# Performance work log

Measured on AMD Instinct MI355X. Metric: run time of the kernel, lower is better.

## Reference

```python
import jax, jax.numpy as jnp
import numpy as np

N_NODES = 50000
N_EDGES = 600000
N_GRAPHS = 100
IN_DIM, HID, OUT = 128, 128, 64
K = 2  # DGL TAGConv default hop count


def setup_inputs() -> dict:
    key = jax.random.key(0)
    ks = jax.random.split(key, 8)
    x = jax.random.normal(ks[0], (N_NODES, IN_DIM), dtype=jnp.float32)
    src = jax.random.randint(ks[1], (N_EDGES,), 0, N_NODES)
    dst = jax.random.randint(ks[2], (N_EDGES,), 0, N_NODES)
    graph_id = jnp.sort(jax.random.randint(ks[3], (N_NODES,), 0, N_GRAPHS))
    # TAGConv lin: Linear(in_feats*(K+1), out_feats), stored as (in*(K+1), out)
    W1 = jax.random.normal(ks[4], (IN_DIM * (K + 1), HID), dtype=jnp.float32) / np.sqrt(IN_DIM * (K + 1))
    b1 = jnp.zeros((HID,), dtype=jnp.float32)
    W2 = jax.random.normal(ks[5], (HID * (K + 1), OUT), dtype=jnp.float32) / np.sqrt(HID * (K + 1))
    b2 = jnp.zeros((OUT,), dtype=jnp.float32)
    return {"x": x, "W1": W1, "b1": b1, "W2": W2, "b2": b2,
            "src": src, "dst": dst, "graph_id": graph_id}


def _tagconv(h, src, dst, norm, W, b):
    """DGL TAGConv: relu(concat_k (D^-1/2 A D^-1/2)^k h @ W + b), k=0..K."""
    feats = [h]
    cur = h
    for _ in range(K):
        cur = cur * norm[:, None]
        cur = jax.ops.segment_sum(cur[src], dst, num_segments=N_NODES)
        cur = cur * norm[:, None]
        feats.append(cur)
    out = jnp.concatenate(feats, axis=-1) @ W + b
    return jax.nn.relu(out)


def reference(x, W1, b1, W2, b2, src, dst, graph_id):
    # symmetric norm from in-degrees (clamped to 1), as in DGL TAGConv
    deg = jax.ops.segment_sum(jnp.ones_like(dst, dtype=x.dtype), dst, num_segments=N_NODES)
    norm = jnp.clip(deg, 1.0, None) ** -0.5
    h = _tagconv(x, src, dst, norm, W1, b1)
    h = _tagconv(h, src, dst, norm, W2, b2)
    # MaxPooling readout: per-graph max over nodes
    return jax.ops.segment_max(h, graph_id, num_segments=N_GRAPHS)
```

## Files before the change

### kernel.cpp

```cpp
#include <hip/hip_runtime.h>
#include <hip/hip_bf16.h>

#define N_NODES 50000
#define N_EDGES 600000
#define N_GRAPHS 100
#define M_PAD 50176

typedef __bf16 bf16_t;
typedef __attribute__((ext_vector_type(8))) __bf16 bf16x8;
typedef __attribute__((ext_vector_type(2))) __bf16 bf16x2;
typedef __attribute__((ext_vector_type(4))) float f32x4;

__global__ void degk(const int* __restrict__ dst, int* __restrict__ deg, int n) {
    int i = blockIdx.x * 256 + threadIdx.x;
    if (i < n) atomicAdd(&deg[dst[i]], 1);
}

__global__ __launch_bounds__(1024) void scan1(const int* __restrict__ deg,
                                              int* __restrict__ row_off,
                                              int* __restrict__ partial,
                                              float* __restrict__ norm, int n) {
    __shared__ int buf[1024];
    int i = blockIdx.x * 1024 + threadIdx.x;
    int v = (i < n) ? deg[i] : 0;
    if (i < n) norm[i] = rsqrtf(fmaxf((float)v, 1.0f));
    buf[threadIdx.x] = v;
    __syncthreads();
    for (int off = 1; off < 1024; off <<= 1) {
        int t = (threadIdx.x >= off) ? buf[threadIdx.x - off] : 0;
        __syncthreads();
        buf[threadIdx.x] += t;
        __syncthreads();
    }
    if (i < n) row_off[i + 1] = buf[threadIdx.x];
    if (threadIdx.x == 1023) partial[blockIdx.x] = buf[1023];
}

__global__ void scan2(int* __restrict__ partial, int nchunks) {
    int lane = threadIdx.x;
    int v = (lane < nchunks) ? partial[lane] : 0;
    for (int off = 1; off < 64; off <<= 1) {
        int t = __shfl_up(v, off, 64);
        if (lane >= off) v += t;
    }
    int ex = __shfl_up(v, 1, 64);
    if (lane == 0) ex = 0;
    if (lane < nchunks) partial[lane] = ex;
}

__global__ void scan3(int* __restrict__ row_off, const int* __restrict__ partial, int n) {
    int i = blockIdx.x * 256 + threadIdx.x;
    if (i == 0) row_off[0] = 0;
    if (i < n) row_off[i + 1] += partial[i >> 10];
}

__global__ void scatterk(const int* __restrict__ src, const int* __restrict__ dst,
                         const int* __restrict__ row_off, int* __restrict__ cursor,
                         int* __restrict__ csr_src, int n) {
    int e = blockIdx.x * 256 + threadIdx.x;
    if (e >= n) return;
    int d = dst[e];
    int pos = atomicAdd(&cursor[d], 1);
    csr_src[row_off[d] + pos] = src[e];
}

__global__ void prescale(const float* __restrict__ x, bf16_t* __restrict__ xb, int n) {
    int i = blockIdx.x * 256 + threadIdx.x;
    if (i >= n * 64) return;
    int node = i >> 6;
    int c = (i & 63) * 2;
    float2 v = *(const float2*)(x + (size_t)node * 128 + c);
    bf16x2 vb; vb[0] = (bf16_t)v.x; vb[1] = (bf16_t)v.y;
    *(bf16x2*)(xb + (size_t)node * 128 + c) = vb;
}

__global__ void permWall(const float* __restrict__ W1, const float* __restrict__ W2,
                         bf16_t* __restrict__ Wp1, bf16_t* __restrict__ Wp2) {
    int i = blockIdx.x * 256 + threadIdx.x;
    const float* W; bf16_t* Wp; int N;
    if (i < 384 * 128) { W = W1; Wp = Wp1; N = 128; }
    else if (i < 384 * 128 + 384 * 64) { i -= 384 * 128; W = W2; Wp = Wp2; N = 64; }
    else return;
    int k = i / N, n = i - k * N;
    int kt = k >> 5, q = (k >> 3) & 3, j = k & 7;
    int nt = n >> 4, ln = n & 15;
    int lane = q * 16 + ln;
    Wp[(((size_t)kt * (N >> 4) + nt) * 64 + lane) * 8 + j] = (bf16_t)W[i];
}

__global__ __launch_bounds__(256) void spmm3(const bf16_t* __restrict__ in,
                                             bf16_t* __restrict__ out,
                                             const float* __restrict__ norm,
                                             const int* __restrict__ row_off,
                                             const int* __restrict__ csr_src, int n) {
    int sub = threadIdx.x >> 4;
    int l   = threadIdx.x & 15;
    int node = blockIdx.x * 16 + sub;
    if (node >= n) return;
    const bf16_t* colp = in + l * 8;
    int e0 = row_off[node], e1 = row_off[node + 1];
    float acc[8] = {};
    int e = e0;
    for (; e + 8 <= e1; e += 8) {
        int s[8];
#pragma unroll
        for (int u = 0; u < 8; u++) s[u] = csr_src[e + u];
        bf16x8 v[8];
#pragma unroll
        for (int u = 0; u < 8; u++) v[u] = *(const bf16x8*)(colp + (size_t)s[u] * 128);
        float ns[8];
#pragma unroll
        for (int u = 0; u < 8; u++) ns[u] = norm[s[u]];
#pragma unroll
        for (int u = 0; u < 8; u++)
#pragma unroll
            for (int j = 0; j < 8; j++) acc[j] += ns[u] * (float)v[u][j];
    }
    for (; e + 4 <= e1; e += 4) {
        int s[4];
#pragma unroll
        for (int u = 0; u < 4; u++) s[u] = csr_src[e + u];
        bf16x8 v[4];
#pragma unroll
        for (int u = 0; u < 4; u++) v[u] = *(const bf16x8*)(colp + (size_t)s[u] * 128);
        float ns[4];
#pragma unroll
        for (int u = 0; u < 4; u++) ns[u] = norm[s[u]];
#pragma unroll
        for (int u = 0; u < 4; u++)
#pragma unroll
            for (int j = 0; j < 8; j++) acc[j] += ns[u] * (float)v[u][j];
    }
    for (; e < e1; e++) {
        int s = csr_src[e];
        float ns = norm[s];
        bf16x8 v = *(const bf16x8*)(colp + (size_t)s * 128);
#pragma unroll
        for (int j = 0; j < 8; j++) acc[j] += ns * (float)v[j];
    }
    float nd = norm[node];
    bf16x8 o;
#pragma unroll
    for (int j = 0; j < 8; j++) o[j] = (bf16_t)(acc[j] * nd);
    *(bf16x8*)(out + (size_t)node * 128 + l * 8) = o;
}

template <int NT, bool BF16OUT>
__global__ __launch_bounds__(256) void gemm_mfma(const bf16_t* __restrict__ f0,
                                                 const bf16_t* __restrict__ f1,
                                                 const bf16_t* __restrict__ f2,
                                                 const bf16_t* __restrict__ Wp,
                                                 const float* __restrict__ bias,
                                                 bf16_t* __restrict__ out_b,
                                                 float* __restrict__ out_f, int M) {
    int wave = threadIdx.x >> 6;
    int lane = threadIdx.x & 63;
    int q = lane >> 4, ln = lane & 15;
    int row0 = blockIdx.x * 128 + wave * 32;

    f32x4 acc[2][NT] = {};
    const bf16_t* feats[3] = {f0, f1, f2};
    const bf16x8* Wf = (const bf16x8*)Wp;

#pragma unroll
    for (int kc = 0; kc < 12; kc++) {
        const bf16_t* A = feats[kc >> 2] + (size_t)(kc & 3) * 32 + q * 8;
        bf16x8 a0 = *(const bf16x8*)(A + (size_t)(row0 + ln) * 128);
        bf16x8 a1 = *(const bf16x8*)(A + (size_t)(row0 + 16 + ln) * 128);
        const bf16x8* Bp = Wf + (size_t)kc * NT * 64 + lane;
#pragma unroll
        for (int nt = 0; nt < NT; nt++) {
            bf16x8 b = Bp[nt * 64];
            acc[0][nt] = __builtin_amdgcn_mfma_f32_16x16x32_bf16(a0, b, acc[0][nt], 0, 0, 0);
            acc[1][nt] = __builtin_amdgcn_mfma_f32_16x16x32_bf16(a1, b, acc[1][nt], 0, 0, 0);
        }
    }

    float bv[NT];
#pragma unroll
    for (int nt = 0; nt < NT; nt++) bv[nt] = bias[nt * 16 + ln];

#pragma unroll
    for (int mt = 0; mt < 2; mt++) {
#pragma unroll
        for (int r = 0; r < 4; r++) {
            int row = row0 + mt * 16 + q * 4 + r;
            if (row >= M) continue;
#pragma unroll
            for (int nt = 0; nt < NT; nt++) {
                int col = nt * 16 + ln;
                float val = fmaxf(acc[mt][nt][r] + bv[nt], 0.f);
                if (BF16OUT) out_b[(size_t)row * 128 + col] = (bf16_t)val;
                else         out_f[(size_t)row * 64 + col] = val;
            }
        }
    }
}

__global__ __launch_bounds__(256) void maxpool2(const float* __restrict__ hF,
                                                const int* __restrict__ gid,
                                                unsigned int* __restrict__ out, int n) {
    int wave = threadIdx.x >> 6;
    int lane = threadIdx.x & 63;
    int n0 = blockIdx.x * 256 + wave * 64;
    if (n0 >= n) return;
    int n1 = min(n0 + 64, n);
    int cur = gid[n0];
    float m = 0.f;
    int i = n0;
    for (; i + 4 <= n1; i += 4) {
        int g0 = gid[i + 0], g1 = gid[i + 1], g2 = gid[i + 2], g3 = gid[i + 3];
        float v0 = hF[(size_t)(i + 0) * 64 + lane];
        float v1 = hF[(size_t)(i + 1) * 64 + lane];
        float v2 = hF[(size_t)(i + 2) * 64 + lane];
        float v3 = hF[(size_t)(i + 3) * 64 + lane];
        if (g0 != cur) { atomicMax(&out[cur * 64 + lane], __float_as_uint(m)); cur = g0; m = v0; } else m = fmaxf(m, v0);
        if (g1 != cur) { atomicMax(&out[cur * 64 + lane], __float_as_uint(m)); cur = g1; m = v1; } else m = fmaxf(m, v1);
        if (g2 != cur) { atomicMax(&out[cur * 64 + lane], __float_as_uint(m)); cur = g2; m = v2; } else m = fmaxf(m, v2);
        if (g3 != cur) { atomicMax(&out[cur * 64 + lane], __float_as_uint(m)); cur = g3; m = v3; } else m = fmaxf(m, v3);
    }
    for (; i < n1; i++) {
        int g = gid[i];
        float v = hF[(size_t)i * 64 + lane];
        if (g != cur) { atomicMax(&out[cur * 64 + lane], __float_as_uint(m)); cur = g; m = v; }
        else m = fmaxf(m, v);
    }
    atomicMax(&out[cur * 64 + lane], __float_as_uint(m));
}

extern "C" void kernel_launch(void* const* d_in, const int* in_sizes, int n_in,
                              void* d_out, int out_size, void* d_ws, size_t ws_size,
                              hipStream_t stream) {
    const float* x  = (const float*)d_in[0];
    const float* W1 = (const float*)d_in[1];
    const float* b1 = (const float*)d_in[2];
    const float* W2 = (const float*)d_in[3];
    const float* b2 = (const float*)d_in[4];
    const int* src  = (const int*)d_in[5];
    const int* dst  = (const int*)d_in[6];
    const int* gid  = (const int*)d_in[7];
    float* out = (float*)d_out;

    char* ws = (char*)d_ws;
    size_t off = 0;
    auto take = [&](size_t bytes) {
        void* p = ws + off;
        off = (off + bytes + 255) & ~(size_t)255;
        return p;
    };
    int* deg     = (int*)take((size_t)N_NODES * 4);
    int* cursor  = (int*)take((size_t)N_NODES * 4);
    size_t zero_bytes = off;
    float* norm  = (float*)take((size_t)N_NODES * 4);
    int* row_off = (int*)take((size_t)(N_NODES + 1) * 4);
    int* partial = (int*)take(64 * 4);
    int* csr_src = (int*)take((size_t)N_EDGES * 4);
    bf16_t* Wp1  = (bf16_t*)take((size_t)384 * 128 * 2);
    bf16_t* Wp2  = (bf16_t*)take((size_t)384 * 64 * 2);
    bf16_t* B0 = (bf16_t*)take((size_t)M_PAD * 128 * 2);
    bf16_t* B1 = (bf16_t*)take((size_t)M_PAD * 128 * 2);
    bf16_t* B2 = (bf16_t*)take((size_t)M_PAD * 128 * 2);
    bf16_t* B3 = (bf16_t*)take((size_t)M_PAD * 128 * 2);
    bf16_t* B5 = (bf16_t*)take((size_t)M_PAD * 128 * 2);
    (void)ws_size; (void)in_sizes; (void)n_in; (void)out_size;

    hipMemsetAsync(d_ws, 0, zero_bytes, stream);
    hipMemsetAsync(d_out, 0, (size_t)N_GRAPHS * 64 * 4, stream);

    degk<<<(N_EDGES + 255) / 256, 256, 0, stream>>>(dst, deg, N_EDGES);

    int nchunks = (N_NODES + 1023) / 1024;
    scan1<<<nchunks, 1024, 0, stream>>>(deg, row_off, partial, norm, N_NODES);
    scan2<<<1, 64, 0, stream>>>(partial, nchunks);
    scan3<<<(N_NODES + 255) / 256, 256, 0, stream>>>(row_off, partial, N_NODES);
    scatterk<<<(N_EDGES + 255) / 256, 256, 0, stream>>>(src, dst, row_off, cursor, csr_src, N_EDGES);

    prescale<<<(N_NODES * 64 + 255) / 256, 256, 0, stream>>>(x, B0, N_NODES);
    permWall<<<(384 * 192 + 255) / 256, 256, 0, stream>>>(W1, W2, Wp1, Wp2);

    int spmm_grid = (N_NODES + 15) / 16;
    int gemm_grid = M_PAD / 128;
    spmm3<<<spmm_grid, 256, 0, stream>>>(B0, B2, norm, row_off, csr_src, N_NODES);
    spmm3<<<spmm_grid, 256, 0, stream>>>(B2, B3, norm, row_off, csr_src, N_NODES);
    gemm_mfma<8, true><<<gemm_grid, 256, 0, stream>>>(B0, B2, B3, Wp1, b1, B5, nullptr, N_NODES);
    spmm3<<<spmm_grid, 256, 0, stream>>>(B5, B2, norm, row_off, csr_src, N_NODES);
    spmm3<<<spmm_grid, 256, 0, stream>>>(B2, B3, norm, row_off, csr_src, N_NODES);
    gemm_mfma<4, false><<<gemm_grid, 256, 0, stream>>>(B5, B2, B3, Wp2, b2, nullptr, (float*)B1, N_NODES);
    maxpool2<<<(N_NODES + 255) / 256, 256, 0, stream>>>((const float*)B1, gid, (unsigned int*)out, N_NODES);
}
```

Before: 314.4 us.

## Store node features in 32-column panels and split SpMM by column group

Feature buffers switch from row-major 128-wide rows to four panels of 32 columns each, with each panel contiguous over nodes. The SpMM now assigns each block one column panel for 64 nodes, so the working set each gather touches is a quarter of the feature matrix and can stay resident in cache. CSR index loads use nontemporal hints, and the GEMM A-loads and bf16 epilogue are rewritten for the panel layout. In exchange, every CSR row, index and norm value is read four times, and each gather becomes a 64-byte segment.

```diff
diff --git a/kernel.cpp b/kernel.cpp
--- a/kernel.cpp
+++ b/kernel.cpp
@@ -5,6 +5,7 @@
 #define N_EDGES 600000
 #define N_GRAPHS 100
 #define M_PAD 50176
+#define PSTR (M_PAD * 32)
 
 typedef __bf16 bf16_t;
 typedef __attribute__((ext_vector_type(8))) __bf16 bf16x8;
@@ -71,7 +72,7 @@
     int c = (i & 63) * 2;
     float2 v = *(const float2*)(x + (size_t)node * 128 + c);
     bf16x2 vb; vb[0] = (bf16_t)v.x; vb[1] = (bf16_t)v.y;
-    *(bf16x2*)(xb + (size_t)node * 128 + c) = vb;
+    *(bf16x2*)(xb + (size_t)(c >> 5) * PSTR + (size_t)node * 32 + (c & 31)) = vb;
 }
 
 __global__ void permWall(const float* __restrict__ W1, const float* __restrict__ W2,
@@ -88,26 +89,28 @@
     Wp[(((size_t)kt * (N >> 4) + nt) * 64 + lane) * 8 + j] = (bf16_t)W[i];
 }
 
-__global__ __launch_bounds__(256) void spmm3(const bf16_t* __restrict__ in,
+__global__ __launch_bounds__(256) void spmm4(const bf16_t* __restrict__ in,
                                              bf16_t* __restrict__ out,
                                              const float* __restrict__ norm,
                                              const int* __restrict__ row_off,
                                              const int* __restrict__ csr_src, int n) {
-    int sub = threadIdx.x >> 4;
-    int l   = threadIdx.x & 15;
-    int node = blockIdx.x * 16 + sub;
+    int cg    = blockIdx.x & 3;
+    int chunk = blockIdx.x >> 2;
+    int sub = threadIdx.x >> 2;
+    int l   = threadIdx.x & 3;
+    int node = chunk * 64 + sub;
     if (node >= n) return;
-    const bf16_t* colp = in + l * 8;
+    const bf16_t* panel = in + (size_t)cg * PSTR + l * 8;
     int e0 = row_off[node], e1 = row_off[node + 1];
     float acc[8] = {};
     int e = e0;
     for (; e + 8 <= e1; e += 8) {
         int s[8];
 #pragma unroll
-        for (int u = 0; u < 8; u++) s[u] = csr_src[e + u];
+        for (int u = 0; u < 8; u++) s[u] = __builtin_nontemporal_load(csr_src + e + u);
         bf16x8 v[8];
 #pragma unroll
-        for (int u = 0; u < 8; u++) v[u] = *(const bf16x8*)(colp + (size_t)s[u] * 128);
+        for (int u = 0; u < 8; u++) v[u] = *(const bf16x8*)(panel + (size_t)s[u] * 32);
         float ns[8];
 #pragma unroll
         for (int u = 0; u < 8; u++) ns[u] = norm[s[u]];
@@ -119,10 +122,10 @@
     for (; e + 4 <= e1; e += 4) {
         int s[4];
 #pragma unroll
-        for (int u = 0; u < 4; u++) s[u] = csr_src[e + u];
+        for (int u = 0; u < 4; u++) s[u] = __builtin_nontemporal_load(csr_src + e + u);
         bf16x8 v[4];
 #pragma unroll
-        for (int u = 0; u < 4; u++) v[u] = *(const bf16x8*)(colp + (size_t)s[u] * 128);
+        for (int u = 0; u < 4; u++) v[u] = *(const bf16x8*)(panel + (size_t)s[u] * 32);
         float ns[4];
 #pragma unroll
         for (int u = 0; u < 4; u++) ns[u] = norm[s[u]];
@@ -132,9 +135,9 @@
             for (int j = 0; j < 8; j++) acc[j] += ns[u] * (float)v[u][j];
     }
     for (; e < e1; e++) {
-        int s = csr_src[e];
+        int s = __builtin_nontemporal_load(csr_src + e);
         float ns = norm[s];
-        bf16x8 v = *(const bf16x8*)(colp + (size_t)s * 128);
+        bf16x8 v = *(const bf16x8*)(panel + (size_t)s * 32);
 #pragma unroll
         for (int j = 0; j < 8; j++) acc[j] += ns * (float)v[j];
     }
@@ -142,7 +145,7 @@
     bf16x8 o;
 #pragma unroll
     for (int j = 0; j < 8; j++) o[j] = (bf16_t)(acc[j] * nd);
-    *(bf16x8*)(out + (size_t)node * 128 + l * 8) = o;
+    *(bf16x8*)(out + (size_t)cg * PSTR + (size_t)node * 32 + l * 8) = o;
 }
 
 template <int NT, bool BF16OUT>
@@ -164,9 +167,9 @@
 
 #pragma unroll
     for (int kc = 0; kc < 12; kc++) {
-        const bf16_t* A = feats[kc >> 2] + (size_t)(kc & 3) * 32 + q * 8;
-        bf16x8 a0 = *(const bf16x8*)(A + (size_t)(row0 + ln) * 128);
-        bf16x8 a1 = *(const bf16x8*)(A + (size_t)(row0 + 16 + ln) * 128);
+        const bf16_t* A = feats[kc >> 2] + (size_t)(kc & 3) * PSTR + q * 8;
+        bf16x8 a0 = *(const bf16x8*)(A + (size_t)(row0 + ln) * 32);
+        bf16x8 a1 = *(const bf16x8*)(A + (size_t)(row0 + 16 + ln) * 32);
         const bf16x8* Bp = Wf + (size_t)kc * NT * 64 + lane;
 #pragma unroll
         for (int nt = 0; nt < NT; nt++) {
@@ -188,10 +191,12 @@
             if (row >= M) continue;
 #pragma unroll
             for (int nt = 0; nt < NT; nt++) {
-                int col = nt * 16 + ln;
                 float val = fmaxf(acc[mt][nt][r] + bv[nt], 0.f);
-                if (BF16OUT) out_b[(size_t)row * 128 + col] = (bf16_t)val;
-                else         out_f[(size_t)row * 64 + col] = val;
+                if (BF16OUT) {
+                    out_b[(size_t)(nt >> 1) * PSTR + (size_t)row * 32 + (nt & 1) * 16 + ln] = (bf16_t)val;
+                } else {
+                    out_f[(size_t)row * 64 + nt * 16 + ln] = val;
+                }
             }
         }
     }
@@ -278,13 +283,13 @@
     prescale<<<(N_NODES * 64 + 255) / 256, 256, 0, stream>>>(x, B0, N_NODES);
     permWall<<<(384 * 192 + 255) / 256, 256, 0, stream>>>(W1, W2, Wp1, Wp2);
 
-    int spmm_grid = (N_NODES + 15) / 16;
+    int spmm_grid = ((N_NODES + 63) / 64) * 4;
     int gemm_grid = M_PAD / 128;
-    spmm3<<<spmm_grid, 256, 0, stream>>>(B0, B2, norm, row_off, csr_src, N_NODES);
-    spmm3<<<spmm_grid, 256, 0, stream>>>(B2, B3, norm, row_off, csr_src, N_NODES);
+    spmm4<<<spmm_grid, 256, 0, stream>>>(B0, B2, norm, row_off, csr_src, N_NODES);
+    spmm4<<<spmm_grid, 256, 0, stream>>>(B2, B3, norm, row_off, csr_src, N_NODES);
     gemm_mfma<8, true><<<gemm_grid, 256, 0, stream>>>(B0, B2, B3, Wp1, b1, B5, nullptr, N_NODES);
-    spmm3<<<spmm_grid, 256, 0, stream>>>(B5, B2, norm, row_off, csr_src, N_NODES);
-    spmm3<<<spmm_grid, 256, 0, stream>>>(B2, B3, norm, row_off, csr_src, N_NODES);
+    spmm4<<<spmm_grid, 256, 0, stream>>>(B5, B2, norm, row_off, csr_src, N_NODES);
+    spmm4<<<spmm_grid, 256, 0, stream>>>(B2, B3, norm, row_off, csr_src, N_NODES);
     gemm_mfma<4, false><<<gemm_grid, 256, 0, stream>>>(B5, B2, B3, Wp2, b2, nullptr, (float*)B1, N_NODES);
     maxpool2<<<(N_NODES + 255) / 256, 256, 0, stream>>>((const float*)B1, gid, (unsigned int*)out, N_NODES);
 }
```

After: 374.0 us. +19.0%, slower.
